# Kernel tuning notes

Measured on AMD Instinct MI355X. Metric: run time of the kernel, lower is better.

## Reference

```python
import jax, jax.numpy as jnp
import numpy as np

B, T1, H, P, V = 4096, 65, 64, 50, 32
D = H + P  # input_size = 114


def setup_inputs() -> dict:
    key = jax.random.key(0)
    ks = jax.random.split(key, 20)
    s = 1.0 / np.sqrt(D)
    sh = 1.0 / np.sqrt(H)
    inp = {
        "phonetic_input": jax.random.normal(ks[0], (B, P), dtype=jnp.float32),
        "char_seq": jax.random.randint(ks[1], (B, T1), 0, V, dtype=jnp.int64),
        "emb": jax.random.normal(ks[2], (V, H), dtype=jnp.float32).at[0].set(0.0),  # padding_idx=0
        "W_rx": jax.random.uniform(ks[3], (D, H), jnp.float32, -s, s),
        "b_rx": jax.random.uniform(ks[4], (H,), jnp.float32, -s, s),
        "W_rh": jax.random.uniform(ks[5], (H, H), jnp.float32, -sh, sh),
        "b_rh": jax.random.uniform(ks[6], (H,), jnp.float32, -sh, sh),
        "W_zx": jax.random.uniform(ks[7], (D, H), jnp.float32, -s, s),
        "b_zx": jax.random.uniform(ks[8], (H,), jnp.float32, -s, s),
        "W_zh": jax.random.uniform(ks[9], (H, H), jnp.float32, -sh, sh),
        "b_zh": jax.random.uniform(ks[10], (H,), jnp.float32, -sh, sh),
        "W_hx": jax.random.uniform(ks[11], (D, H), jnp.float32, -s, s),
        "b_hx": jax.random.uniform(ks[12], (H,), jnp.float32, -s, s),
        "W_hh": jax.random.uniform(ks[13], (H, H), jnp.float32, -sh, sh),
        "b_hh": jax.random.uniform(ks[14], (H,), jnp.float32, -sh, sh),
        "W_proj": jax.random.uniform(ks[15], (H, V), jnp.float32, -sh, sh),
        "b_proj": jax.random.uniform(ks[16], (V,), jnp.float32, -sh, sh),
    }
    return inp


def reference(phonetic_input, char_seq, emb, W_rx, b_rx, W_rh, b_rh, W_zx, b_zx,
              W_zh, b_zh, W_hx, b_hx, W_hh, b_hh, W_proj, b_proj):
    input_seq = char_seq[:, :-1]          # [B, T]
    target_seq = char_seq[:, 1:]          # [B, T]
    Bsz, T = input_seq.shape

    char_emb = emb[input_seq]                                   # [B, T, H]
    phon = jnp.broadcast_to(phonetic_input[:, None, :], (Bsz, T, P))
    x = jnp.concatenate([char_emb, phon], axis=2)               # [B, T, D]

    # Hoist input-side projections into batched GEMMs, [T, B, H] for scan
    xr = jnp.einsum('btd,dh->tbh', x, W_rx) + b_rx
    xz = jnp.einsum('btd,dh->tbh', x, W_zx) + b_zx
    xh = jnp.einsum('btd,dh->tbh', x, W_hx) + b_hx

    h0 = jnp.zeros((Bsz, H), dtype=x.dtype)

    def step(h, inputs):
        xr_t, xz_t, xh_t = inputs
        r = jax.nn.sigmoid(xr_t + h @ W_rh + b_rh)
        z = jax.nn.sigmoid(xz_t + h @ W_zh + b_zh)
        c = jnp.tanh(xh_t + (r * h) @ W_hh + b_hh)
        h_new = (1.0 - z) * h + z * c
        return h_new, h_new

    _, hs = jax.lax.scan(step, h0, (xr, xz, xh))                # [T, B, H]
    logits = jnp.einsum('tbh,hv->btv', hs, W_proj) + b_proj     # [B, T, V]

    # cross_entropy with ignore_index=0 (mean over non-ignored)
    targets = target_seq.reshape(-1)
    logp = jax.nn.log_softmax(logits.reshape(-1, V), axis=-1)
    nll = -jnp.take_along_axis(logp, targets[:, None], axis=-1)[:, 0]
    mask = (targets != 0).astype(logits.dtype)
    loss = jnp.sum(nll * mask) / jnp.maximum(jnp.sum(mask), 1.0)
    return logits, loss
```

## Files before the change

kernel.cpp:

```cpp
#include <hip/hip_runtime.h>
#include <stdint.h>

#define Bsz 4096
#define Tn  64
#define T1n 65
#define Hn  64
#define Pn  50
#define Vn  32

typedef __attribute__((ext_vector_type(8))) short short8;
typedef __attribute__((ext_vector_type(4))) float floatx4;

__device__ __forceinline__ float bf2f(unsigned short u) {
  union { unsigned int i; float f; } x; x.i = ((unsigned int)u) << 16; return x.f;
}
__device__ __forceinline__ unsigned short f2bf(float f) {
  union { float f; unsigned int i; } x; x.f = f;
  return (unsigned short)((x.i + 0x7FFFu + ((x.i >> 16) & 1u)) >> 16);
}
__device__ __forceinline__ float fast_sigmoid(float x) {
  return __builtin_amdgcn_rcpf(1.f + __expf(-x));
}
__device__ __forceinline__ float fast_tanh(float x) {
  return 1.f - 2.f * __builtin_amdgcn_rcpf(1.f + __expf(2.f * x));
}

__device__ __forceinline__ short8 load_bfrag(const float* __restrict__ W, int ncols, int col, int kbase) {
  short8 f;
#pragma unroll
  for (int j = 0; j < 8; ++j) f[j] = (short)f2bf(W[(long)(kbase + j) * ncols + col]);
  return f;
}

__launch_bounds__(512)
__global__ void gru_kernel(const float* __restrict__ phon,
                           const int* __restrict__ cs,
                           const float* __restrict__ emb,
                           const float* __restrict__ Wrx, const float* __restrict__ brx,
                           const float* __restrict__ Wrh, const float* __restrict__ brh,
                           const float* __restrict__ Wzx, const float* __restrict__ bzx,
                           const float* __restrict__ Wzh, const float* __restrict__ bzh,
                           const float* __restrict__ Whx, const float* __restrict__ bhx,
                           const float* __restrict__ Whh, const float* __restrict__ bhh,
                           const float* __restrict__ Wpj, const float* __restrict__ bpj_g,
                           float* __restrict__ ws,
                           float* __restrict__ outp) {
  __shared__ unsigned short tbl_s[3 * 32 * 66];
  __shared__ __align__(16) unsigned short hist_s[8 * 1152];
  __shared__ __align__(16) unsigned short rh_s[1152];
  __shared__ float logit_s[9 * 16 * 33];
  __shared__ unsigned int code4_s[(T1n + 1) * 4];
  __shared__ int det_s[1];
  __shared__ float red_s[16];

  const int tid = threadIdx.x;
  const int b0 = blockIdx.x * 16;
  const int W8 = tid >> 6, lane = tid & 63, q = lane >> 4, c16 = lane & 15;
  const bool isScan = (W8 < 4);
  const int w = isScan ? W8 : (W8 - 4);
  const int jcol = w * 16 + c16;
  const floatx4 zf = {0.f, 0.f, 0.f, 0.f};

  if (tid == 0) det_s[0] = 0;
  __syncthreads();
  if (tid < 128 && cs[2 * tid + 1] != 0) atomicOr(&det_s[0], 1);
  __syncthreads();
  const bool is64 = (det_s[0] == 0);

  for (int i = tid; i < 1152; i += 512) hist_s[7 * 1152 + i] = 0;
  for (int i = tid; i < T1n * 4; i += 512) {
    int t = i >> 2, qq = i & 3;
    unsigned int pk = 0;
#pragma unroll
    for (int r = 0; r < 4; ++r) {
      long idx = (long)(b0 + qq * 4 + r) * T1n + t;
      int c = is64 ? cs[2 * idx] : cs[idx];
      pk |= ((unsigned int)(c & 255)) << (8 * r);
    }
    code4_s[i] = pk;
  }

  for (int g = 0; g < 3; ++g) {
    const float* Wg = (g == 0) ? Wrx : (g == 1) ? Wzx : Whx;
    const float* bx = (g == 0) ? brx : (g == 1) ? bzx : bhx;
    const float* bh = (g == 0) ? brh : (g == 1) ? bzh : bhh;
    float acc[4] = {0.f, 0.f, 0.f, 0.f};
    float bias = bx[lane] + bh[lane];
    for (int d = 0; d < Hn; ++d) {
      float wv = Wg[(long)d * Hn + lane];
#pragma unroll
      for (int k = 0; k < 4; ++k)
        acc[k] += emb[(long)(W8 + 8 * k) * Hn + d] * wv;
    }
#pragma unroll
    for (int k = 0; k < 4; ++k)
      tbl_s[g * 2112 + (W8 + 8 * k) * 66 + lane] = f2bf(acc[k] + bias);
  }

  float ph_r[4] = {0.f, 0.f, 0.f, 0.f};
  float ph_z[4] = {0.f, 0.f, 0.f, 0.f};
  float ph_h[4] = {0.f, 0.f, 0.f, 0.f};
  if (isScan) {
    for (int p = 0; p < Pn; ++p) {
      float wr = Wrx[(long)(Hn + p) * Hn + jcol];
      float wz = Wzx[(long)(Hn + p) * Hn + jcol];
      float wh = Whx[(long)(Hn + p) * Hn + jcol];
#pragma unroll
      for (int r = 0; r < 4; ++r) {
        float xv = phon[(long)(b0 + q * 4 + r) * Pn + p];
        ph_r[r] += xv * wr; ph_z[r] += xv * wz; ph_h[r] += xv * wh;
      }
    }
  }

  short8 Br0, Br1, Bz0, Bz1, Bh0, Bh1;
  short8 Bp0, Bp1;
  float bpj = 0.f;
  if (isScan) {
    Br0 = load_bfrag(Wrh, Hn, jcol, q * 8);
    Br1 = load_bfrag(Wrh, Hn, jcol, 32 + q * 8);
    Bz0 = load_bfrag(Wzh, Hn, jcol, q * 8);
    Bz1 = load_bfrag(Wzh, Hn, jcol, 32 + q * 8);
    Bh0 = load_bfrag(Whh, Hn, jcol, q * 8);
    Bh1 = load_bfrag(Whh, Hn, jcol, 32 + q * 8);
    Bp0 = Br0; Bp1 = Br1;
  } else if (W8 < 6) {
    int vt = W8 - 4;
    Bp0 = load_bfrag(Wpj, Vn, vt * 16 + c16, q * 8);
    Bp1 = load_bfrag(Wpj, Vn, vt * 16 + c16, 32 + q * 8);
    bpj = bpj_g[vt * 16 + c16];
    Br0 = Bp0; Br1 = Bp1; Bz0 = Bp0; Bz1 = Bp1; Bh0 = Bp0; Bh1 = Bp1;
  } else {
    short8 zs = {0,0,0,0,0,0,0,0};
    Br0 = zs; Br1 = zs; Bz0 = zs; Bz1 = zs; Bh0 = zs; Bh1 = zs; Bp0 = zs; Bp1 = zs;
  }

  float h[4] = {0.f, 0.f, 0.f, 0.f};
  float z4[4] = {0.f, 0.f, 0.f, 0.f};
  float nll = 0.f, cnt = 0.f;
  int pp = 0;

  __syncthreads();

  for (int t = 0; t < Tn; ++t) {
    const unsigned int pk = code4_s[t * 4 + q];
    unsigned short tc[4];
    if (isScan) {
      const unsigned short* hp = &hist_s[((t + 7) & 7) * 1152];
      short8 a0 = *(const short8*)&hp[c16 * 72 + q * 8];
      short8 a1 = *(const short8*)&hp[c16 * 72 + 32 + q * 8];
      floatx4 accr = __builtin_amdgcn_mfma_f32_16x16x32_bf16(a0, Br0, zf, 0, 0, 0);
      floatx4 accz = __builtin_amdgcn_mfma_f32_16x16x32_bf16(a0, Bz0, zf, 0, 0, 0);
      accr = __builtin_amdgcn_mfma_f32_16x16x32_bf16(a1, Br1, accr, 0, 0, 0);
      accz = __builtin_amdgcn_mfma_f32_16x16x32_bf16(a1, Bz1, accz, 0, 0, 0);
#pragma unroll
      for (int r = 0; r < 4; ++r) {
        int cr = (pk >> (8 * r)) & 255;
        tc[r] = tbl_s[2 * 2112 + cr * 66 + jcol];
        float xr = bf2f(tbl_s[0 * 2112 + cr * 66 + jcol]) + ph_r[r] + accr[r];
        float xz = bf2f(tbl_s[1 * 2112 + cr * 66 + jcol]) + ph_z[r] + accz[r];
        z4[r] = fast_sigmoid(xz);
        rh_s[(q * 4 + r) * 72 + jcol] = f2bf(fast_sigmoid(xr) * h[r]);
      }
    } else if (W8 < 6 && t > 0) {
      const unsigned short* hp = &hist_s[((t + 7) & 7) * 1152];
      short8 a0 = *(const short8*)&hp[c16 * 72 + q * 8];
      short8 a1 = *(const short8*)&hp[c16 * 72 + 32 + q * 8];
      floatx4 l = __builtin_amdgcn_mfma_f32_16x16x32_bf16(a0, Bp0, zf, 0, 0, 0);
      l = __builtin_amdgcn_mfma_f32_16x16x32_bf16(a1, Bp1, l, 0, 0, 0);
      float* pg = &logit_s[pp * 528];
      int vt = W8 - 4;
#pragma unroll
      for (int r = 0; r < 4; ++r)
        pg[(q * 4 + r) * 33 + vt * 16 + c16] = l[r] + bpj;
      pp = (pp == 8) ? 0 : pp + 1;
    }
    __syncthreads();

    if (isScan) {
      short8 p0 = *(const short8*)&rh_s[c16 * 72 + q * 8];
      short8 p1 = *(const short8*)&rh_s[c16 * 72 + 32 + q * 8];
      floatx4 acc = __builtin_amdgcn_mfma_f32_16x16x32_bf16(p0, Bh0, zf, 0, 0, 0);
      acc = __builtin_amdgcn_mfma_f32_16x16x32_bf16(p1, Bh1, acc, 0, 0, 0);
      unsigned short* hw = &hist_s[(t & 7) * 1152];
#pragma unroll
      for (int r = 0; r < 4; ++r) {
        float xh = bf2f(tc[r]) + ph_h[r] + acc[r];
        float c = fast_tanh(xh);
        float hn = fmaf(z4[r], c - h[r], h[r]);
        h[r] = hn;
        hw[(q * 4 + r) * 72 + jcol] = f2bf(hn);
      }
    }
    __syncthreads();

    if ((t & 7) == 7) {
      int p = t - 8 + W8;
      if (p >= 0) {
        const float* pg = &logit_s[(p % 9) * 528];
        int v = lane & 31, hf = lane >> 5;
#pragma unroll
        for (int i = 0; i < 8; ++i) {
          int m = i * 2 + hf;
          float lg = pg[m * 33 + v];
          float s = __expf(lg);
#pragma unroll
          for (int off = 16; off >= 1; off >>= 1) s += __shfl_xor(s, off);
          float lse = __logf(s);
          outp[(((long)(b0 + m)) * Tn + p) * Vn + v] = lg;
          unsigned int pk1 = code4_s[(p + 1) * 4 + (m >> 2)];
          int targ = (pk1 >> (8 * (m & 3))) & 255;
          if (targ != 0 && v == targ) { nll += lse - lg; cnt += 1.f; }
        }
      }
    }
  }

  if (W8 >= 4 && W8 < 6) {
    const unsigned short* hp = &hist_s[7 * 1152];
    short8 a0 = *(const short8*)&hp[c16 * 72 + q * 8];
    short8 a1 = *(const short8*)&hp[c16 * 72 + 32 + q * 8];
    floatx4 l = __builtin_amdgcn_mfma_f32_16x16x32_bf16(a0, Bp0, zf, 0, 0, 0);
    l = __builtin_amdgcn_mfma_f32_16x16x32_bf16(a1, Bp1, l, 0, 0, 0);
    int vt = W8 - 4;
#pragma unroll
    for (int r = 0; r < 4; ++r)
      logit_s[0 * 528 + (q * 4 + r) * 33 + vt * 16 + c16] = l[r] + bpj;
  }
  __syncthreads();
  if (W8 == 0) {
    const float* pg = &logit_s[0 * 528];
    int v = lane & 31, hf = lane >> 5;
#pragma unroll
    for (int i = 0; i < 8; ++i) {
      int m = i * 2 + hf;
      float lg = pg[m * 33 + v];
      float s = __expf(lg);
#pragma unroll
      for (int off = 16; off >= 1; off >>= 1) s += __shfl_xor(s, off);
      float lse = __logf(s);
      outp[(((long)(b0 + m)) * Tn + 63) * Vn + v] = lg;
      unsigned int pk1 = code4_s[64 * 4 + (m >> 2)];
      int targ = (pk1 >> (8 * (m & 3))) & 255;
      if (targ != 0 && v == targ) { nll += lse - lg; cnt += 1.f; }
    }
  }

#pragma unroll
  for (int off = 32; off >= 1; off >>= 1) {
    nll += __shfl_xor(nll, off);
    cnt += __shfl_xor(cnt, off);
  }
  if (lane == 0) { red_s[W8] = nll; red_s[8 + W8] = cnt; }
  __syncthreads();
  if (tid == 0) {
    float n = 0.f, c = 0.f;
#pragma unroll
    for (int i = 0; i < 8; ++i) { n += red_s[i]; c += red_s[8 + i]; }
    ws[2 * blockIdx.x] = n;
    ws[2 * blockIdx.x + 1] = c;
  }
}

__global__ void loss_kernel(const float* __restrict__ ws, float* __restrict__ outp) {
  int lane = threadIdx.x;
  float n = 0.f, c = 0.f;
  for (int i = lane; i < Bsz / 16; i += 64) { n += ws[2 * i]; c += ws[2 * i + 1]; }
#pragma unroll
  for (int off = 32; off >= 1; off >>= 1) {
    n += __shfl_xor(n, off);
    c += __shfl_xor(c, off);
  }
  if (lane == 0) outp[(size_t)Bsz * Tn * Vn] = n / fmaxf(c, 1.f);
}

extern "C" void kernel_launch(void* const* d_in, const int* in_sizes, int n_in,
                              void* d_out, int out_size, void* d_ws, size_t ws_size,
                              hipStream_t stream) {
  const float* phon = (const float*)d_in[0];
  const int*   cs   = (const int*)d_in[1];
  const float* emb  = (const float*)d_in[2];
  const float* Wrx  = (const float*)d_in[3];
  const float* brx  = (const float*)d_in[4];
  const float* Wrh  = (const float*)d_in[5];
  const float* brh  = (const float*)d_in[6];
  const float* Wzx  = (const float*)d_in[7];
  const float* bzx  = (const float*)d_in[8];
  const float* Wzh  = (const float*)d_in[9];
  const float* bzh  = (const float*)d_in[10];
  const float* Whx  = (const float*)d_in[11];
  const float* bhx  = (const float*)d_in[12];
  const float* Whh  = (const float*)d_in[13];
  const float* bhh  = (const float*)d_in[14];
  const float* Wpj  = (const float*)d_in[15];
  const float* bpj  = (const float*)d_in[16];
  float* ws = (float*)d_ws;

  hipLaunchKernelGGL(gru_kernel, dim3(Bsz / 16), dim3(512), 0, stream,
                     phon, cs, emb, Wrx, brx, Wrh, brh, Wzx, bzx, Wzh, bzh,
                     Whx, bhx, Whh, bhh, Wpj, bpj, ws, (float*)d_out);
  hipLaunchKernelGGL(loss_kernel, dim3(1), dim3(64), 0, stream, ws, (float*)d_out);
}
```

Measured before the change: 170.2 us.

## Shrink GRU block to 5 waves with a single projection wave and inline loss

Cuts the block from 8 waves to 5. One wave now computes both 16-column projection tiles and does the softmax/NLL straight from registers at each step, which removes the logit staging buffer, the 8-deep history ring (now double-buffered) and the periodic batched loss phase. Barriers become a custom s_waitcnt lgkmcnt(0) plus s_barrier. The aims are lower LDS use and fewer waves per block so more blocks fit, less barrier overhead and no bursty loss work. The cost is that the single projection wave may now sit on the per-step critical path with global stores and exps.

```diff
diff --git a/kernel.cpp b/kernel.cpp
--- a/kernel.cpp
+++ b/kernel.cpp
@@ -8,6 +8,9 @@
 #define Pn  50
 #define Vn  32
 
+#define NW  5
+#define NT  320
+
 typedef __attribute__((ext_vector_type(8))) short short8;
 typedef __attribute__((ext_vector_type(4))) float floatx4;
 
@@ -24,6 +27,9 @@
 __device__ __forceinline__ float fast_tanh(float x) {
   return 1.f - 2.f * __builtin_amdgcn_rcpf(1.f + __expf(2.f * x));
 }
+__device__ __forceinline__ void bar_lgkm() {
+  asm volatile("s_waitcnt lgkmcnt(0)\n\ts_barrier" ::: "memory");
+}
 
 __device__ __forceinline__ short8 load_bfrag(const float* __restrict__ W, int ncols, int col, int kbase) {
   short8 f;
@@ -32,7 +38,7 @@
   return f;
 }
 
-__launch_bounds__(512)
+__launch_bounds__(NT)
 __global__ void gru_kernel(const float* __restrict__ phon,
                            const int* __restrict__ cs,
                            const float* __restrict__ emb,
@@ -46,19 +52,16 @@
                            float* __restrict__ ws,
                            float* __restrict__ outp) {
   __shared__ unsigned short tbl_s[3 * 32 * 66];
-  __shared__ __align__(16) unsigned short hist_s[8 * 1152];
+  __shared__ __align__(16) unsigned short hist_s[2 * 1152];
   __shared__ __align__(16) unsigned short rh_s[1152];
-  __shared__ float logit_s[9 * 16 * 33];
   __shared__ unsigned int code4_s[(T1n + 1) * 4];
   __shared__ int det_s[1];
-  __shared__ float red_s[16];
 
   const int tid = threadIdx.x;
   const int b0 = blockIdx.x * 16;
   const int W8 = tid >> 6, lane = tid & 63, q = lane >> 4, c16 = lane & 15;
   const bool isScan = (W8 < 4);
-  const int w = isScan ? W8 : (W8 - 4);
-  const int jcol = w * 16 + c16;
+  const int jcol = W8 * 16 + c16;
   const floatx4 zf = {0.f, 0.f, 0.f, 0.f};
 
   if (tid == 0) det_s[0] = 0;
@@ -67,8 +70,8 @@
   __syncthreads();
   const bool is64 = (det_s[0] == 0);
 
-  for (int i = tid; i < 1152; i += 512) hist_s[7 * 1152 + i] = 0;
-  for (int i = tid; i < T1n * 4; i += 512) {
+  for (int i = tid; i < 1152; i += NT) hist_s[1152 + i] = 0;
+  for (int i = tid; i < T1n * 4; i += NT) {
     int t = i >> 2, qq = i & 3;
     unsigned int pk = 0;
 #pragma unroll
@@ -84,17 +87,21 @@
     const float* Wg = (g == 0) ? Wrx : (g == 1) ? Wzx : Whx;
     const float* bx = (g == 0) ? brx : (g == 1) ? bzx : bhx;
     const float* bh = (g == 0) ? brh : (g == 1) ? bzh : bhh;
-    float acc[4] = {0.f, 0.f, 0.f, 0.f};
+    float acc[7] = {0.f, 0.f, 0.f, 0.f, 0.f, 0.f, 0.f};
     float bias = bx[lane] + bh[lane];
     for (int d = 0; d < Hn; ++d) {
       float wv = Wg[(long)d * Hn + lane];
 #pragma unroll
-      for (int k = 0; k < 4; ++k)
-        acc[k] += emb[(long)(W8 + 8 * k) * Hn + d] * wv;
-    }
-#pragma unroll
-    for (int k = 0; k < 4; ++k)
-      tbl_s[g * 2112 + (W8 + 8 * k) * 66 + lane] = f2bf(acc[k] + bias);
+      for (int k = 0; k < 7; ++k) {
+        int v = W8 + NW * k;
+        if (v < 32) acc[k] += emb[(long)v * Hn + d] * wv;
+      }
+    }
+#pragma unroll
+    for (int k = 0; k < 7; ++k) {
+      int v = W8 + NW * k;
+      if (v < 32) tbl_s[g * 2112 + v * 66 + lane] = f2bf(acc[k] + bias);
+    }
   }
 
   float ph_r[4] = {0.f, 0.f, 0.f, 0.f};
@@ -113,9 +120,9 @@
     }
   }
 
-  short8 Br0, Br1, Bz0, Bz1, Bh0, Bh1;
-  short8 Bp0, Bp1;
-  float bpj = 0.f;
+  short8 Br0 = {0,0,0,0,0,0,0,0}, Br1 = Br0, Bz0 = Br0, Bz1 = Br0, Bh0 = Br0, Bh1 = Br0;
+  short8 Bp00 = Br0, Bp01 = Br0, Bp10 = Br0, Bp11 = Br0;
+  float bpj0 = 0.f, bpj1 = 0.f;
   if (isScan) {
     Br0 = load_bfrag(Wrh, Hn, jcol, q * 8);
     Br1 = load_bfrag(Wrh, Hn, jcol, 32 + q * 8);
@@ -123,30 +130,28 @@
     Bz1 = load_bfrag(Wzh, Hn, jcol, 32 + q * 8);
     Bh0 = load_bfrag(Whh, Hn, jcol, q * 8);
     Bh1 = load_bfrag(Whh, Hn, jcol, 32 + q * 8);
-    Bp0 = Br0; Bp1 = Br1;
-  } else if (W8 < 6) {
-    int vt = W8 - 4;
-    Bp0 = load_bfrag(Wpj, Vn, vt * 16 + c16, q * 8);
-    Bp1 = load_bfrag(Wpj, Vn, vt * 16 + c16, 32 + q * 8);
-    bpj = bpj_g[vt * 16 + c16];
-    Br0 = Bp0; Br1 = Bp1; Bz0 = Bp0; Bz1 = Bp1; Bh0 = Bp0; Bh1 = Bp1;
   } else {
-    short8 zs = {0,0,0,0,0,0,0,0};
-    Br0 = zs; Br1 = zs; Bz0 = zs; Bz1 = zs; Bh0 = zs; Bh1 = zs; Bp0 = zs; Bp1 = zs;
+    Bp00 = load_bfrag(Wpj, Vn, c16,      q * 8);
+    Bp01 = load_bfrag(Wpj, Vn, c16,      32 + q * 8);
+    Bp10 = load_bfrag(Wpj, Vn, 16 + c16, q * 8);
+    Bp11 = load_bfrag(Wpj, Vn, 16 + c16, 32 + q * 8);
+    bpj0 = bpj_g[c16];
+    bpj1 = bpj_g[16 + c16];
   }
 
   float h[4] = {0.f, 0.f, 0.f, 0.f};
   float z4[4] = {0.f, 0.f, 0.f, 0.f};
   float nll = 0.f, cnt = 0.f;
-  int pp = 0;
 
   __syncthreads();
 
   for (int t = 0; t < Tn; ++t) {
     const unsigned int pk = code4_s[t * 4 + q];
     unsigned short tc[4];
+    float lg0[4], lg1[4], e0[4], e1[4];
+
     if (isScan) {
-      const unsigned short* hp = &hist_s[((t + 7) & 7) * 1152];
+      const unsigned short* hp = &hist_s[((t + 1) & 1) * 1152];
       short8 a0 = *(const short8*)&hp[c16 * 72 + q * 8];
       short8 a1 = *(const short8*)&hp[c16 * 72 + 32 + q * 8];
       floatx4 accr = __builtin_amdgcn_mfma_f32_16x16x32_bf16(a0, Br0, zf, 0, 0, 0);
@@ -162,27 +167,34 @@
         z4[r] = fast_sigmoid(xz);
         rh_s[(q * 4 + r) * 72 + jcol] = f2bf(fast_sigmoid(xr) * h[r]);
       }
-    } else if (W8 < 6 && t > 0) {
-      const unsigned short* hp = &hist_s[((t + 7) & 7) * 1152];
+    } else if (t > 0) {
+      const unsigned short* hp = &hist_s[((t + 1) & 1) * 1152];
       short8 a0 = *(const short8*)&hp[c16 * 72 + q * 8];
       short8 a1 = *(const short8*)&hp[c16 * 72 + 32 + q * 8];
-      floatx4 l = __builtin_amdgcn_mfma_f32_16x16x32_bf16(a0, Bp0, zf, 0, 0, 0);
-      l = __builtin_amdgcn_mfma_f32_16x16x32_bf16(a1, Bp1, l, 0, 0, 0);
-      float* pg = &logit_s[pp * 528];
-      int vt = W8 - 4;
-#pragma unroll
-      for (int r = 0; r < 4; ++r)
-        pg[(q * 4 + r) * 33 + vt * 16 + c16] = l[r] + bpj;
-      pp = (pp == 8) ? 0 : pp + 1;
-    }
-    __syncthreads();
+      floatx4 l0 = __builtin_amdgcn_mfma_f32_16x16x32_bf16(a0, Bp00, zf, 0, 0, 0);
+      floatx4 l1 = __builtin_amdgcn_mfma_f32_16x16x32_bf16(a0, Bp10, zf, 0, 0, 0);
+      l0 = __builtin_amdgcn_mfma_f32_16x16x32_bf16(a1, Bp01, l0, 0, 0, 0);
+      l1 = __builtin_amdgcn_mfma_f32_16x16x32_bf16(a1, Bp11, l1, 0, 0, 0);
+      const int p = t - 1;
+#pragma unroll
+      for (int r = 0; r < 4; ++r) {
+        lg0[r] = l0[r] + bpj0;
+        lg1[r] = l1[r] + bpj1;
+        long ad = ((long)(b0 + q * 4 + r)) * ((long)Tn * Vn) + (long)p * Vn;
+        outp[ad + c16]      = lg0[r];
+        outp[ad + 16 + c16] = lg1[r];
+        e0[r] = __expf(lg0[r]);
+        e1[r] = __expf(lg1[r]);
+      }
+    }
+    bar_lgkm();
 
     if (isScan) {
       short8 p0 = *(const short8*)&rh_s[c16 * 72 + q * 8];
       short8 p1 = *(const short8*)&rh_s[c16 * 72 + 32 + q * 8];
       floatx4 acc = __builtin_amdgcn_mfma_f32_16x16x32_bf16(p0, Bh0, zf, 0, 0, 0);
       acc = __builtin_amdgcn_mfma_f32_16x16x32_bf16(p1, Bh1, acc, 0, 0, 0);
-      unsigned short* hw = &hist_s[(t & 7) * 1152];
+      unsigned short* hw = &hist_s[(t & 1) * 1152];
 #pragma unroll
       for (int r = 0; r < 4; ++r) {
         float xh = bf2f(tc[r]) + ph_h[r] + acc[r];
@@ -191,74 +203,57 @@
         h[r] = hn;
         hw[(q * 4 + r) * 72 + jcol] = f2bf(hn);
       }
-    }
-    __syncthreads();
-
-    if ((t & 7) == 7) {
-      int p = t - 8 + W8;
-      if (p >= 0) {
-        const float* pg = &logit_s[(p % 9) * 528];
-        int v = lane & 31, hf = lane >> 5;
-#pragma unroll
-        for (int i = 0; i < 8; ++i) {
-          int m = i * 2 + hf;
-          float lg = pg[m * 33 + v];
-          float s = __expf(lg);
-#pragma unroll
-          for (int off = 16; off >= 1; off >>= 1) s += __shfl_xor(s, off);
-          float lse = __logf(s);
-          outp[(((long)(b0 + m)) * Tn + p) * Vn + v] = lg;
-          unsigned int pk1 = code4_s[(p + 1) * 4 + (m >> 2)];
-          int targ = (pk1 >> (8 * (m & 3))) & 255;
-          if (targ != 0 && v == targ) { nll += lse - lg; cnt += 1.f; }
+    } else if (t > 0) {
+#pragma unroll
+      for (int r = 0; r < 4; ++r) {
+        float s = e0[r] + e1[r];
+        s += __shfl_xor(s, 1); s += __shfl_xor(s, 2);
+        s += __shfl_xor(s, 4); s += __shfl_xor(s, 8);
+        float lse = __logf(s);
+        int targ = (pk >> (8 * r)) & 255;
+        if (targ != 0) {
+          if (c16 == targ)           { nll += lse - lg0[r]; cnt += 1.f; }
+          else if (c16 + 16 == targ) { nll += lse - lg1[r]; cnt += 1.f; }
         }
       }
     }
-  }
-
-  if (W8 >= 4 && W8 < 6) {
-    const unsigned short* hp = &hist_s[7 * 1152];
+    bar_lgkm();
+  }
+
+  if (W8 == 4) {
+    const unsigned short* hp = &hist_s[1 * 1152];
     short8 a0 = *(const short8*)&hp[c16 * 72 + q * 8];
     short8 a1 = *(const short8*)&hp[c16 * 72 + 32 + q * 8];
-    floatx4 l = __builtin_amdgcn_mfma_f32_16x16x32_bf16(a0, Bp0, zf, 0, 0, 0);
-    l = __builtin_amdgcn_mfma_f32_16x16x32_bf16(a1, Bp1, l, 0, 0, 0);
-    int vt = W8 - 4;
-#pragma unroll
-    for (int r = 0; r < 4; ++r)
-      logit_s[0 * 528 + (q * 4 + r) * 33 + vt * 16 + c16] = l[r] + bpj;
-  }
-  __syncthreads();
-  if (W8 == 0) {
-    const float* pg = &logit_s[0 * 528];
-    int v = lane & 31, hf = lane >> 5;
-#pragma unroll
-    for (int i = 0; i < 8; ++i) {
-      int m = i * 2 + hf;
-      float lg = pg[m * 33 + v];
-      float s = __expf(lg);
-#pragma unroll
-      for (int off = 16; off >= 1; off >>= 1) s += __shfl_xor(s, off);
+    floatx4 l0 = __builtin_amdgcn_mfma_f32_16x16x32_bf16(a0, Bp00, zf, 0, 0, 0);
+    floatx4 l1 = __builtin_amdgcn_mfma_f32_16x16x32_bf16(a0, Bp10, zf, 0, 0, 0);
+    l0 = __builtin_amdgcn_mfma_f32_16x16x32_bf16(a1, Bp01, l0, 0, 0, 0);
+    l1 = __builtin_amdgcn_mfma_f32_16x16x32_bf16(a1, Bp11, l1, 0, 0, 0);
+    const unsigned int pk = code4_s[64 * 4 + q];
+#pragma unroll
+    for (int r = 0; r < 4; ++r) {
+      float g0 = l0[r] + bpj0, g1 = l1[r] + bpj1;
+      long ad = ((long)(b0 + q * 4 + r)) * ((long)Tn * Vn) + (long)63 * Vn;
+      outp[ad + c16]      = g0;
+      outp[ad + 16 + c16] = g1;
+      float s = __expf(g0) + __expf(g1);
+      s += __shfl_xor(s, 1); s += __shfl_xor(s, 2);
+      s += __shfl_xor(s, 4); s += __shfl_xor(s, 8);
       float lse = __logf(s);
-      outp[(((long)(b0 + m)) * Tn + 63) * Vn + v] = lg;
-      unsigned int pk1 = code4_s[64 * 4 + (m >> 2)];
-      int targ = (pk1 >> (8 * (m & 3))) & 255;
-      if (targ != 0 && v == targ) { nll += lse - lg; cnt += 1.f; }
-    }
-  }
-
-#pragma unroll
-  for (int off = 32; off >= 1; off >>= 1) {
-    nll += __shfl_xor(nll, off);
-    cnt += __shfl_xor(cnt, off);
-  }
-  if (lane == 0) { red_s[W8] = nll; red_s[8 + W8] = cnt; }
-  __syncthreads();
-  if (tid == 0) {
-    float n = 0.f, c = 0.f;
-#pragma unroll
-    for (int i = 0; i < 8; ++i) { n += red_s[i]; c += red_s[8 + i]; }
-    ws[2 * blockIdx.x] = n;
-    ws[2 * blockIdx.x + 1] = c;
+      int targ = (pk >> (8 * r)) & 255;
+      if (targ != 0) {
+        if (c16 == targ)           { nll += lse - g0; cnt += 1.f; }
+        else if (c16 + 16 == targ) { nll += lse - g1; cnt += 1.f; }
+      }
+    }
+#pragma unroll
+    for (int off = 32; off >= 1; off >>= 1) {
+      nll += __shfl_xor(nll, off);
+      cnt += __shfl_xor(cnt, off);
+    }
+    if (lane == 0) {
+      ws[2 * blockIdx.x] = nll;
+      ws[2 * blockIdx.x + 1] = cnt;
+    }
   }
 }
 
@@ -296,7 +291,7 @@
   const float* bpj  = (const float*)d_in[16];
   float* ws = (float*)d_ws;
 
-  hipLaunchKernelGGL(gru_kernel, dim3(Bsz / 16), dim3(512), 0, stream,
+  hipLaunchKernelGGL(gru_kernel, dim3(Bsz / 16), dim3(NT), 0, stream,
                      phon, cs, emb, Wrx, brx, Wrh, brh, Wzx, bzx, Wzh, bzh,
                      Whx, bhx, Whh, bhh, Wpj, bpj, ws, (float*)d_out);
   hipLaunchKernelGGL(loss_kernel, dim3(1), dim3(64), 0, stream, ws, (float*)d_out);
```

Result: slower. 271.7 us (+59.6%).
